# Kernel optimization log

Hardware: AMD Instinct MI355X
Metric: run time of the kernel (lower is better)

The kernel has to match this reference:

```python
import jax, jax.numpy as jnp
import numpy as np


def _hippo_scale_params(N, L):
    """Replicates HiPPOScale.__init__ for discretization='bilinear' (pure numpy)."""
    q = np.arange(N, dtype=np.float64)
    col, row = np.meshgrid(q, q)
    r = 2 * q + 1
    M = -(np.where(row >= col, r, 0) - np.diag(q))
    T = np.sqrt(np.diag(2 * q + 1))
    A = T @ M @ np.linalg.inv(T)          # (N, N)
    B = np.diag(T)                         # (N,)
    ts = np.arange(1, L + 1, dtype=np.float64)[:, None, None]  # (L,1,1)
    At = A[None] / ts                      # A / t, batched over t
    I = np.eye(N, dtype=np.float64)
    Mm = I[None] - 0.5 * At
    Nn = I[None] + 0.5 * At
    A_stacked = np.linalg.solve(Mm, Nn)                      # (L, N, N)
    Bt = B[None, :] / ts[:, 0, :]                             # (L, N)
    B_stacked = np.linalg.solve(Mm, Bt[..., None])[..., 0]    # (L, N)
    return A_stacked.astype(np.float32), B_stacked.astype(np.float32)


def setup_inputs() -> dict:
    N, L, Bsz = 64, 4096, 64
    key = jax.random.key(0)
    A_st, B_st = _hippo_scale_params(N, L)
    inputs = jax.random.normal(key, (L, Bsz), dtype=jnp.float32)
    return {
        "inputs": inputs,                       # (L, B)
        "A_stacked": jnp.asarray(A_st),         # (L, N, N)
        "B_stacked": jnp.asarray(B_st),         # (L, N)
    }


def reference(inputs, A_stacked, B_stacked):
    # u[t, b, :] = inputs[t, b] * B_stacked[t, :]   -> (L, B, N)
    u = inputs[..., None] * B_stacked[:, None, :]

    # x[t] = A[t] @ x[t-1] + u[t], x[-1] = 0  (time-varying linear recurrence).
    # The torch code computes this via a divide-and-conquer unroll; here we use
    # the equivalent parallel associative scan with elements (A, u) and
    # composition (A2@A1, A2@u1 + u2).
    def combine(e1, e2):
        a1, u1 = e1
        a2, u2 = e2
        a = jnp.matmul(a2, a1)                                  # (l, N, N)
        v = jnp.einsum('...ij,...bj->...bi', a2, u1) + u2       # (l, B, N)
        return (a, v)

    _, x = jax.lax.associative_scan(combine, (A_stacked, u))
    return x  # (L, B, N)
```

## Files before the change

kernel.cpp:

```cpp
#include <hip/hip_runtime.h>
#include <hip/hip_bf16.h>

#define TL 4096
#define NB 64
#define CH 8
#define CN 512
#define AS 72

typedef __attribute__((ext_vector_type(8))) short short8;
typedef __attribute__((ext_vector_type(4))) short short4v;
typedef __attribute__((ext_vector_type(4))) float floatx4;
typedef __attribute__((ext_vector_type(4))) unsigned int uint4v;

__device__ inline floatx4 mfma_bf16(short8 a, short8 b, floatx4 c) {
    return __builtin_amdgcn_mfma_f32_16x16x32_bf16(a, b, c, 0, 0, 0);
}

__device__ inline short bf16_rne(float x) {
    union { __hip_bfloat16 b; unsigned short s; } u;
    u.b = __float2bfloat16(x);
    return (short)u.s;
}

__device__ inline void split_bf16(float x, short& h, short& l) {
    h = bf16_rne(x);
    union { unsigned u; float f; } hv; hv.u = ((unsigned)(unsigned short)h) << 16;
    l = bf16_rne(x - hv.f);
}

__global__ __launch_bounds__(256, 2)
void hippo_phase1(const float* __restrict__ inp, const float* __restrict__ Ag,
                  const float* __restrict__ Bst,
                  unsigned* __restrict__ P32, float* __restrict__ VT)
{
    __shared__ short Ah[NB][AS], Al[NB][AS];
    __shared__ short SBh[NB][AS], SBl[NB][AS];
    __shared__ short VBh[NB][AS], VBl[NB][AS];
    __shared__ float btl[NB], itl[NB];

    const int tid  = threadIdx.x;
    const int c    = blockIdx.x;
    const int t0   = c * CH;
    const int w    = tid >> 6, lane = tid & 63;
    const int quad = lane >> 4, l15 = lane & 15;

#pragma unroll
    for (int q = 0; q < 16; ++q) {
        int f = tid + q * 256;
        int n = f >> 6, k = f & 63;
        SBh[n][k] = (n == k) ? (short)0x3F80 : (short)0;
        SBl[n][k] = 0; VBh[n][k] = 0; VBl[n][k] = 0;
    }

    float4 pre[4];
    {
        const float4* Ap = (const float4*)(Ag + (size_t)t0 * 4096);
#pragma unroll
        for (int q = 0; q < 4; ++q) pre[q] = Ap[tid + q * 256];
    }

    floatx4 accS[4], accV[4];

    for (int s = 0; s < CH; ++s) {
        int t = t0 + s;
#pragma unroll
        for (int q = 0; q < 4; ++q) {
            int f = tid + q * 256;
            int m = f >> 4, k0 = (f & 15) * 4;
            float vv[4] = {pre[q].x, pre[q].y, pre[q].z, pre[q].w};
            short4v h4, l4;
#pragma unroll
            for (int r = 0; r < 4; ++r) { short hh, ll; split_bf16(vv[r], hh, ll); h4[r]=hh; l4[r]=ll; }
            *(short4v*)&Ah[m][k0] = h4;
            *(short4v*)&Al[m][k0] = l4;
        }
        if (tid < 64) { btl[tid] = Bst[(size_t)t*64 + tid]; itl[tid] = inp[(size_t)t*64 + tid]; }
        if (s + 1 < CH) {
            const float4* Ap = (const float4*)(Ag + (size_t)(t+1) * 4096);
#pragma unroll
            for (int q = 0; q < 4; ++q) pre[q] = Ap[tid + q * 256];
        }
        __syncthreads();

#pragma unroll
        for (int ni = 0; ni < 4; ++ni) {
            float ib = itl[16*ni + l15];
#pragma unroll
            for (int r = 0; r < 4; ++r) {
                accS[ni][r] = 0.0f;
                accV[ni][r] = btl[16*w + 4*quad + r] * ib;
            }
        }
#pragma unroll
        for (int kc = 0; kc < 2; ++kc) {
            int ko = 32*kc + 8*quad;
            short8 aH = *(const short8*)&Ah[16*w + l15][ko];
            short8 aL = *(const short8*)&Al[16*w + l15][ko];
#pragma unroll
            for (int ni = 0; ni < 4; ++ni) {
                int n = 16*ni + l15;
                short8 sH = *(const short8*)&SBh[n][ko];
                short8 sL = *(const short8*)&SBl[n][ko];
                accS[ni] = mfma_bf16(aH, sH, accS[ni]);
                accS[ni] = mfma_bf16(aH, sL, accS[ni]);
                accS[ni] = mfma_bf16(aL, sH, accS[ni]);
                short8 vH = *(const short8*)&VBh[n][ko];
                short8 vL = *(const short8*)&VBl[n][ko];
                accV[ni] = mfma_bf16(aH, vH, accV[ni]);
                accV[ni] = mfma_bf16(aH, vL, accV[ni]);
                accV[ni] = mfma_bf16(aL, vH, accV[ni]);
            }
        }
        __syncthreads();

        if (s + 1 < CH) {
#pragma unroll
            for (int ni = 0; ni < 4; ++ni) {
                int cc = 16*ni + l15, r0 = 16*w + 4*quad;
                short4v h4, l4;
#pragma unroll
                for (int r = 0; r < 4; ++r) { short hh,ll; split_bf16(accS[ni][r],hh,ll); h4[r]=hh; l4[r]=ll; }
                *(short4v*)&SBh[cc][r0] = h4; *(short4v*)&SBl[cc][r0] = l4;
#pragma unroll
                for (int r = 0; r < 4; ++r) { short hh,ll; split_bf16(accV[ni][r],hh,ll); h4[r]=hh; l4[r]=ll; }
                *(short4v*)&VBh[cc][r0] = h4; *(short4v*)&VBl[cc][r0] = l4;
            }
        }
    }
    unsigned* po = P32 + (size_t)c * 4096;
#pragma unroll
    for (int ni = 0; ni < 4; ++ni) {
        int cc = 16*ni + l15, r0 = 16*w + 4*quad;
        *(floatx4*)(VT + (size_t)c*4096 + cc*64 + r0) = accV[ni];
#pragma unroll
        for (int r = 0; r < 4; ++r) {
            short hh, ll; split_bf16(accS[ni][r], hh, ll);
            po[(r0 + r)*64 + cc] = ((unsigned)(unsigned short)hh << 16) | (unsigned)(unsigned short)ll;
        }
    }
}

__global__ __launch_bounds__(256, 2)
void hippo_seqscan(unsigned* __restrict__ P32, float* __restrict__ VT,
                   int bstride, int off0, int estride)
{
    __shared__ short PAh[NB][AS], PAl[NB][AS];
    __shared__ short PBh[NB][AS], PBl[NB][AS];
    __shared__ short VBh[NB][AS], VBl[NB][AS];

    const int tid  = threadIdx.x;
    const int base = blockIdx.x * bstride + off0;
    const int w    = tid >> 6, lane = tid & 63;
    const int quad = lane >> 4, l15 = lane & 15;

    {
        const unsigned* p0 = P32 + (size_t)base * 4096;
        const float*    v0 = VT  + (size_t)base * 4096;
#pragma unroll
        for (int q = 0; q < 4; ++q) {
            int f = tid + q * 256;
            int k = f & 63, m0 = (f >> 6) * 4;
            uint4v pk = *(const uint4v*)(p0 + k * 64 + m0);
#pragma unroll
            for (int r = 0; r < 4; ++r) {
                PBh[m0 + r][k] = (short)(pk[r] >> 16);
                PBl[m0 + r][k] = (short)(pk[r] & 0xFFFFu);
            }
        }
#pragma unroll
        for (int q = 0; q < 4; ++q) {
            int f = tid + q * 256;
            int n = f >> 4, k0 = (f & 15) * 4;
            float4 vv = *(const float4*)(v0 + n * 64 + k0);
            float va[4] = {vv.x, vv.y, vv.z, vv.w};
            short4v vh4, vl4;
#pragma unroll
            for (int r = 0; r < 4; ++r) { short hh, ll; split_bf16(va[r], hh, ll); vh4[r]=hh; vl4[r]=ll; }
            *(short4v*)&VBh[n][k0] = vh4; *(short4v*)&VBl[n][k0] = vl4;
        }
    }

    uint4v preA[4]; float4 preV[4];
    {
        const unsigned* pc = P32 + (size_t)(base + estride) * 4096;
        const float*    vc = VT  + (size_t)(base + estride) * 4096;
#pragma unroll
        for (int q = 0; q < 4; ++q) {
            int f = tid + q * 256;
            int m = f >> 4, k0 = (f & 15) * 4;
            preA[q] = *(const uint4v*)(pc + m * 64 + k0);
        }
#pragma unroll
        for (int ni = 0; ni < 4; ++ni) {
            int cc = 16 * ni + l15, r0 = 16 * w + 4 * quad;
            preV[ni] = *(const float4*)(vc + cc * 64 + r0);
        }
    }

    for (int i = 1; i < 8; ++i) {
#pragma unroll
        for (int q = 0; q < 4; ++q) {
            int f = tid + q * 256;
            int m = f >> 4, k0 = (f & 15) * 4;
            short4v h4, l4;
#pragma unroll
            for (int r = 0; r < 4; ++r) { h4[r] = (short)(preA[q][r] >> 16); l4[r] = (short)(preA[q][r] & 0xFFFFu); }
            *(short4v*)&PAh[m][k0] = h4;
            *(short4v*)&PAl[m][k0] = l4;
        }
        floatx4 accP[4], accV[4];
#pragma unroll
        for (int ni = 0; ni < 4; ++ni) {
            accV[ni][0] = preV[ni].x; accV[ni][1] = preV[ni].y;
            accV[ni][2] = preV[ni].z; accV[ni][3] = preV[ni].w;
            accP[ni][0] = accP[ni][1] = accP[ni][2] = accP[ni][3] = 0.0f;
        }
        if (i + 1 < 8) {
            const unsigned* pc = P32 + (size_t)(base + (i + 1) * estride) * 4096;
            const float*    vc = VT  + (size_t)(base + (i + 1) * estride) * 4096;
#pragma unroll
            for (int q = 0; q < 4; ++q) {
                int f = tid + q * 256;
                int m = f >> 4, k0 = (f & 15) * 4;
                preA[q] = *(const uint4v*)(pc + m * 64 + k0);
            }
#pragma unroll
            for (int ni = 0; ni < 4; ++ni) {
                int cc = 16 * ni + l15, r0 = 16 * w + 4 * quad;
                preV[ni] = *(const float4*)(vc + cc * 64 + r0);
            }
        }
        __syncthreads();

#pragma unroll
        for (int kc = 0; kc < 2; ++kc) {
            int ko = 32 * kc + 8 * quad;
            short8 aH = *(const short8*)&PAh[16 * w + l15][ko];
            short8 aL = *(const short8*)&PAl[16 * w + l15][ko];
#pragma unroll
            for (int ni = 0; ni < 4; ++ni) {
                int n = 16 * ni + l15;
                short8 pH = *(const short8*)&PBh[n][ko];
                short8 pL = *(const short8*)&PBl[n][ko];
                accP[ni] = mfma_bf16(aH, pH, accP[ni]);
                accP[ni] = mfma_bf16(aH, pL, accP[ni]);
                accP[ni] = mfma_bf16(aL, pH, accP[ni]);
                short8 vH = *(const short8*)&VBh[n][ko];
                short8 vL = *(const short8*)&VBl[n][ko];
                accV[ni] = mfma_bf16(aH, vH, accV[ni]);
                accV[ni] = mfma_bf16(aH, vL, accV[ni]);
                accV[ni] = mfma_bf16(aL, vH, accV[ni]);
            }
        }
        __syncthreads();

        int idx = base + i * estride;
        unsigned* po = P32 + (size_t)idx * 4096;
#pragma unroll
        for (int ni = 0; ni < 4; ++ni) {
            int cc = 16 * ni + l15, r0 = 16 * w + 4 * quad;
            *(floatx4*)(VT + (size_t)idx * 4096 + cc * 64 + r0) = accV[ni];
            short4v h4, l4;
#pragma unroll
            for (int r = 0; r < 4; ++r) {
                short hh, ll; split_bf16(accP[ni][r], hh, ll);
                po[(r0 + r) * 64 + cc] = ((unsigned)(unsigned short)hh << 16) | (unsigned)(unsigned short)ll;
                h4[r] = hh; l4[r] = ll;
            }
            *(short4v*)&PBh[cc][r0] = h4; *(short4v*)&PBl[cc][r0] = l4;
#pragma unroll
            for (int r = 0; r < 4; ++r) { short hh,ll; split_bf16(accV[ni][r],hh,ll); h4[r]=hh; l4[r]=ll; }
            *(short4v*)&VBh[cc][r0] = h4; *(short4v*)&VBl[cc][r0] = l4;
        }
    }
}

__global__ __launch_bounds__(256, 2)
void hippo_s3(unsigned* __restrict__ P32, const float* __restrict__ VT)
{
    __shared__ short PAh[NB][AS], PAl[NB][AS];
    __shared__ short EBh[NB][AS], EBl[NB][AS];
    const int tid = threadIdx.x;
    const int w = tid >> 6, lane = tid & 63, quad = lane >> 4, l15 = lane & 15;

#pragma unroll
    for (int q = 0; q < 16; ++q) {
        int f = tid + q * 256; EBh[f >> 6][f & 63] = 0; EBl[f >> 6][f & 63] = 0;
    }
    for (int s = 0; s < 7; ++s) {
        int idx = 64 * s + 63;
        const unsigned* pc = P32 + (size_t)idx * 4096;
        const float*    vc = VT  + (size_t)idx * 4096;
#pragma unroll
        for (int q = 0; q < 4; ++q) {
            int f = tid + q * 256;
            int m = f >> 4, k0 = (f & 15) * 4;
            uint4v pk = *(const uint4v*)(pc + m * 64 + k0);
            short4v h4, l4;
#pragma unroll
            for (int r = 0; r < 4; ++r) { h4[r] = (short)(pk[r] >> 16); l4[r] = (short)(pk[r] & 0xFFFFu); }
            *(short4v*)&PAh[m][k0] = h4;
            *(short4v*)&PAl[m][k0] = l4;
        }
        floatx4 acc[4];
#pragma unroll
        for (int ni = 0; ni < 4; ++ni) {
            int cc = 16 * ni + l15, r0 = 16 * w + 4 * quad;
            float4 vv = *(const float4*)(vc + cc * 64 + r0);
            acc[ni][0] = vv.x; acc[ni][1] = vv.y; acc[ni][2] = vv.z; acc[ni][3] = vv.w;
        }
        __syncthreads();
#pragma unroll
        for (int kc = 0; kc < 2; ++kc) {
            int ko = 32 * kc + 8 * quad;
            short8 aH = *(const short8*)&PAh[16 * w + l15][ko];
            short8 aL = *(const short8*)&PAl[16 * w + l15][ko];
#pragma unroll
            for (int ni = 0; ni < 4; ++ni) {
                int n = 16 * ni + l15;
                short8 eH = *(const short8*)&EBh[n][ko];
                short8 eL = *(const short8*)&EBl[n][ko];
                acc[ni] = mfma_bf16(aH, eH, acc[ni]);
                acc[ni] = mfma_bf16(aH, eL, acc[ni]);
                acc[ni] = mfma_bf16(aL, eH, acc[ni]);
            }
        }
        __syncthreads();
        float* eo = (float*)(P32 + (size_t)idx * 4096);
#pragma unroll
        for (int ni = 0; ni < 4; ++ni) {
            int cc = 16 * ni + l15, r0 = 16 * w + 4 * quad;
            *(floatx4*)(eo + cc * 64 + r0) = acc[ni];
            short4v h4, l4;
#pragma unroll
            for (int r = 0; r < 4; ++r) { short hh,ll; split_bf16(acc[ni][r],hh,ll); h4[r]=hh; l4[r]=ll; }
            *(short4v*)&EBh[cc][r0] = h4; *(short4v*)&EBl[cc][r0] = l4;
        }
    }
}

__global__ __launch_bounds__(256, 2)
void hippo_phase3(const float* __restrict__ inp, const float* __restrict__ Ag,
                  const float* __restrict__ Bst, const unsigned* __restrict__ P32,
                  const float* __restrict__ VT, float* __restrict__ out)
{
    __shared__ short Ah[NB][AS], Al[NB][AS];
    __shared__ short XBh[NB][AS], XBl[NB][AS];
    __shared__ float btl[NB], itl[NB];

    const int tid = threadIdx.x, c = blockIdx.x, t0 = c * CH;
    const int w = tid>>6, lane = tid&63, quad = lane>>4, l15 = lane&15;
    const int sup = c >> 6, g = c >> 3, gi = g & 7, j = c & 7;

    float4 pre[4];
    {
        const float4* Ap = (const float4*)(Ag + (size_t)t0 * 4096);
#pragma unroll
        for (int q = 0; q < 4; ++q) pre[q] = Ap[tid + q * 256];
    }

    if (sup == 0) {
#pragma unroll
        for (int q = 0; q < 16; ++q) { int f = tid + q*256; XBh[f>>6][f&63] = 0; XBl[f>>6][f&63] = 0; }
    } else {
        const float* e = (const float*)(P32 + (size_t)(64*(sup-1) + 63) * 4096);
#pragma unroll
        for (int q = 0; q < 4; ++q) {
            int f = tid + q*256; int b = f>>4, k0 = (f&15)*4;
            float4 v = *(const float4*)(e + b*64 + k0);
            float va[4] = {v.x,v.y,v.z,v.w};
            short4v h4, l4;
#pragma unroll
            for (int r=0;r<4;++r){short hh,ll;split_bf16(va[r],hh,ll);h4[r]=hh;l4[r]=ll;}
            *(short4v*)&XBh[b][k0] = h4; *(short4v*)&XBl[b][k0] = l4;
        }
    }

    auto combine = [&](int idx) {
        const unsigned* pc = P32 + (size_t)idx * 4096;
        const float*    vc = VT  + (size_t)idx * 4096;
#pragma unroll
        for (int q = 0; q < 4; ++q) {
            int f = tid + q*256;
            int m = f >> 4, k0 = (f & 15) * 4;
            uint4v pk = *(const uint4v*)(pc + m * 64 + k0);
            short4v h4, l4;
#pragma unroll
            for (int r = 0; r < 4; ++r) { h4[r] = (short)(pk[r] >> 16); l4[r] = (short)(pk[r] & 0xFFFFu); }
            *(short4v*)&Ah[m][k0] = h4;
            *(short4v*)&Al[m][k0] = l4;
        }
        floatx4 acc[4];
#pragma unroll
        for (int ni = 0; ni < 4; ++ni) {
            int cc = 16*ni + l15, r0 = 16*w + 4*quad;
            float4 vv = *(const float4*)(vc + cc*64 + r0);
            acc[ni][0]=vv.x; acc[ni][1]=vv.y; acc[ni][2]=vv.z; acc[ni][3]=vv.w;
        }
        __syncthreads();
#pragma unroll
        for (int kc = 0; kc < 2; ++kc) {
            int ko = 32*kc + 8*quad;
            short8 aH = *(const short8*)&Ah[16*w + l15][ko];
            short8 aL = *(const short8*)&Al[16*w + l15][ko];
#pragma unroll
            for (int ni = 0; ni < 4; ++ni) {
                int n = 16*ni + l15;
                short8 xH = *(const short8*)&XBh[n][ko];
                short8 xL = *(const short8*)&XBl[n][ko];
                acc[ni] = mfma_bf16(aH, xH, acc[ni]);
                acc[ni] = mfma_bf16(aH, xL, acc[ni]);
                acc[ni] = mfma_bf16(aL, xH, acc[ni]);
            }
        }
        __syncthreads();
#pragma unroll
        for (int ni = 0; ni < 4; ++ni) {
            int cc = 16*ni + l15, r0 = 16*w + 4*quad;
            short4v h4, l4;
#pragma unroll
            for (int r=0;r<4;++r){short hh,ll;split_bf16(acc[ni][r],hh,ll);h4[r]=hh;l4[r]=ll;}
            *(short4v*)&XBh[cc][r0] = h4; *(short4v*)&XBl[cc][r0] = l4;
        }
    };
    if (gi) combine(8*g - 1);
    if (j)  combine(c - 1);

    floatx4 acc[4];
    for (int s = 0; s < CH; ++s) {
        int t = t0 + s;
#pragma unroll
        for (int q = 0; q < 4; ++q) {
            int f = tid + q*256; int m = f>>4, k0 = (f&15)*4;
            float vv[4] = {pre[q].x,pre[q].y,pre[q].z,pre[q].w};
            short4v h4, l4;
#pragma unroll
            for (int r=0;r<4;++r){short hh,ll;split_bf16(vv[r],hh,ll);h4[r]=hh;l4[r]=ll;}
            *(short4v*)&Ah[m][k0] = h4; *(short4v*)&Al[m][k0] = l4;
        }
        if (tid < 64) { btl[tid] = Bst[(size_t)t*64 + tid]; itl[tid] = inp[(size_t)t*64 + tid]; }
        if (s + 1 < CH) {
            const float4* Ap = (const float4*)(Ag + (size_t)(t+1) * 4096);
#pragma unroll
            for (int q = 0; q < 4; ++q) pre[q] = Ap[tid + q * 256];
        }
        __syncthreads();

#pragma unroll
        for (int ni = 0; ni < 4; ++ni) {
            float ib = itl[16*ni + l15];
#pragma unroll
            for (int r = 0; r < 4; ++r) acc[ni][r] = btl[16*w + 4*quad + r] * ib;
        }
#pragma unroll
        for (int kc = 0; kc < 2; ++kc) {
            int ko = 32*kc + 8*quad;
            short8 aH = *(const short8*)&Ah[16*w + l15][ko];
            short8 aL = *(const short8*)&Al[16*w + l15][ko];
#pragma unroll
            for (int ni = 0; ni < 4; ++ni) {
                int n = 16*ni + l15;
                short8 xH = *(const short8*)&XBh[n][ko];
                short8 xL = *(const short8*)&XBl[n][ko];
                acc[ni] = mfma_bf16(aH, xH, acc[ni]);
                acc[ni] = mfma_bf16(aH, xL, acc[ni]);
                acc[ni] = mfma_bf16(aL, xH, acc[ni]);
            }
        }
        __syncthreads();
#pragma unroll
        for (int ni = 0; ni < 4; ++ni) {
            int cc = 16*ni + l15, r0 = 16*w + 4*quad;
            *(floatx4*)(out + (size_t)t*4096 + cc*64 + r0) = acc[ni];
            if (s + 1 < CH) {
                short4v h4, l4;
#pragma unroll
                for (int r=0;r<4;++r){short hh,ll;split_bf16(acc[ni][r],hh,ll);h4[r]=hh;l4[r]=ll;}
                *(short4v*)&XBh[cc][r0] = h4; *(short4v*)&XBl[cc][r0] = l4;
            }
        }
    }
}

extern "C" void kernel_launch(void* const* d_in, const int* in_sizes, int n_in,
                              void* d_out, int out_size, void* d_ws, size_t ws_size,
                              hipStream_t stream)
{
    const float* inp = (const float*)d_in[0];
    const float* A   = (const float*)d_in[1];
    const float* Bst = (const float*)d_in[2];
    float* out = (float*)d_out;
    float* ws  = (float*)d_ws;

    unsigned* P32 = (unsigned*)ws;
    float*    VT  = ws + (size_t)CN * 4096;

    hippo_phase1<<<CN, 256, 0, stream>>>(inp, A, Bst, P32, VT);
    hippo_seqscan<<<64, 256, 0, stream>>>(P32, VT, 8, 0, 1);
    hippo_seqscan<<<8, 256, 0, stream>>>(P32, VT, 64, 7, 8);
    hippo_s3<<<1, 256, 0, stream>>>(P32, VT);
    hippo_phase3<<<CN, 256, 0, stream>>>(inp, A, Bst, P32, VT, out);
}
```

Baseline: 184.0 us.

## Use 2x2 warp tiling, skip identity step, prefetch B/input into registers

Each wave now computes a 32x32 output tile (two M blocks by two N blocks) instead of a 16x64 strip. This halves the redundant B-operand LDS reads per MFMA and lets the A fragments be reused across two column blocks. Phase 1 also skips the first step's multiply by the identity matrix: it loads A[t0] and the first u directly into the accumulators and starts the loop at s=1. The per-step B and input values are now prefetched into registers a step ahead instead of staged through shared memory by one wave. The cost is more live registers per thread and scattered scalar global loads for the initial A.

Measured after the change: 180.1 us. -2.2%, faster.

```diff
diff --git a/kernel.cpp b/kernel.cpp
--- a/kernel.cpp
+++ b/kernel.cpp
@@ -36,105 +36,164 @@
     __shared__ short Ah[NB][AS], Al[NB][AS];
     __shared__ short SBh[NB][AS], SBl[NB][AS];
     __shared__ short VBh[NB][AS], VBl[NB][AS];
-    __shared__ float btl[NB], itl[NB];
-
-    const int tid  = threadIdx.x;
-    const int c    = blockIdx.x;
-    const int t0   = c * CH;
-    const int w    = tid >> 6, lane = tid & 63;
+
+    const int tid = threadIdx.x;
+    const int c = blockIdx.x, t0 = c * CH;
+    const int w = tid >> 6, lane = tid & 63;
     const int quad = lane >> 4, l15 = lane & 15;
-
-#pragma unroll
-    for (int q = 0; q < 16; ++q) {
-        int f = tid + q * 256;
-        int n = f >> 6, k = f & 63;
-        SBh[n][k] = (n == k) ? (short)0x3F80 : (short)0;
-        SBl[n][k] = 0; VBh[n][k] = 0; VBl[n][k] = 0;
+    const int wm = w >> 1, wb = w & 1;
+    const int mr0 = 32*wm, br0 = 32*wb;
+
+    floatx4 accS[2][2], accV[2][2];
+
+    {
+        const float* A0 = Ag + (size_t)t0 * 4096;
+#pragma unroll
+        for (int mi = 0; mi < 2; ++mi) {
+            const int r0 = mr0 + 16*mi + 4*quad;
+            float bt[4];
+#pragma unroll
+            for (int r = 0; r < 4; ++r) bt[r] = Bst[(size_t)t0*64 + r0 + r];
+#pragma unroll
+            for (int ni = 0; ni < 2; ++ni) {
+                const int cc = br0 + 16*ni + l15;
+                const float ii = inp[(size_t)t0*64 + cc];
+#pragma unroll
+                for (int r = 0; r < 4; ++r) {
+                    accS[mi][ni][r] = A0[(size_t)(r0 + r)*64 + cc];
+                    accV[mi][ni][r] = bt[r] * ii;
+                }
+            }
+        }
     }
 
     float4 pre[4];
+    float preB[2][4], preI[2];
     {
-        const float4* Ap = (const float4*)(Ag + (size_t)t0 * 4096);
-#pragma unroll
-        for (int q = 0; q < 4; ++q) pre[q] = Ap[tid + q * 256];
-    }
-
-    floatx4 accS[4], accV[4];
-
-    for (int s = 0; s < CH; ++s) {
-        int t = t0 + s;
-#pragma unroll
-        for (int q = 0; q < 4; ++q) {
-            int f = tid + q * 256;
-            int m = f >> 4, k0 = (f & 15) * 4;
+        const float4* Ap = (const float4*)(Ag + (size_t)(t0+1) * 4096);
+#pragma unroll
+        for (int q = 0; q < 4; ++q) pre[q] = Ap[tid + q*256];
+#pragma unroll
+        for (int mi = 0; mi < 2; ++mi)
+#pragma unroll
+            for (int r = 0; r < 4; ++r)
+                preB[mi][r] = Bst[(size_t)(t0+1)*64 + mr0 + 16*mi + 4*quad + r];
+        preI[0] = inp[(size_t)(t0+1)*64 + br0 + l15];
+        preI[1] = inp[(size_t)(t0+1)*64 + br0 + 16 + l15];
+    }
+
+#pragma unroll
+    for (int mi = 0; mi < 2; ++mi)
+#pragma unroll
+    for (int ni = 0; ni < 2; ++ni) {
+        const int cc = br0 + 16*ni + l15, r0 = mr0 + 16*mi + 4*quad;
+        short4v h4, l4;
+#pragma unroll
+        for (int r = 0; r < 4; ++r) { short hh,ll; split_bf16(accS[mi][ni][r],hh,ll); h4[r]=hh; l4[r]=ll; }
+        *(short4v*)&SBh[cc][r0] = h4; *(short4v*)&SBl[cc][r0] = l4;
+#pragma unroll
+        for (int r = 0; r < 4; ++r) { short hh,ll; split_bf16(accV[mi][ni][r],hh,ll); h4[r]=hh; l4[r]=ll; }
+        *(short4v*)&VBh[cc][r0] = h4; *(short4v*)&VBl[cc][r0] = l4;
+    }
+
+    for (int s = 1; s < CH; ++s) {
+#pragma unroll
+        for (int q = 0; q < 4; ++q) {
+            int f = tid + q*256;
+            int m = f >> 4, k0 = (f & 15)*4;
             float vv[4] = {pre[q].x, pre[q].y, pre[q].z, pre[q].w};
             short4v h4, l4;
 #pragma unroll
-            for (int r = 0; r < 4; ++r) { short hh, ll; split_bf16(vv[r], hh, ll); h4[r]=hh; l4[r]=ll; }
-            *(short4v*)&Ah[m][k0] = h4;
-            *(short4v*)&Al[m][k0] = l4;
-        }
-        if (tid < 64) { btl[tid] = Bst[(size_t)t*64 + tid]; itl[tid] = inp[(size_t)t*64 + tid]; }
+            for (int r = 0; r < 4; ++r) { short hh,ll; split_bf16(vv[r],hh,ll); h4[r]=hh; l4[r]=ll; }
+            *(short4v*)&Ah[m][k0] = h4; *(short4v*)&Al[m][k0] = l4;
+        }
+        float bcur[2][4], icur[2];
+#pragma unroll
+        for (int mi=0;mi<2;++mi)
+#pragma unroll
+            for (int r=0;r<4;++r) bcur[mi][r] = preB[mi][r];
+        icur[0]=preI[0]; icur[1]=preI[1];
         if (s + 1 < CH) {
-            const float4* Ap = (const float4*)(Ag + (size_t)(t+1) * 4096);
-#pragma unroll
-            for (int q = 0; q < 4; ++q) pre[q] = Ap[tid + q * 256];
-        }
-        __syncthreads();
-
-#pragma unroll
-        for (int ni = 0; ni < 4; ++ni) {
-            float ib = itl[16*ni + l15];
-#pragma unroll
-            for (int r = 0; r < 4; ++r) {
-                accS[ni][r] = 0.0f;
-                accV[ni][r] = btl[16*w + 4*quad + r] * ib;
-            }
+            const int t1 = t0 + s + 1;
+            const float4* Ap = (const float4*)(Ag + (size_t)t1 * 4096);
+#pragma unroll
+            for (int q = 0; q < 4; ++q) pre[q] = Ap[tid + q*256];
+#pragma unroll
+            for (int mi=0;mi<2;++mi)
+#pragma unroll
+                for (int r=0;r<4;++r)
+                    preB[mi][r] = Bst[(size_t)t1*64 + mr0 + 16*mi + 4*quad + r];
+            preI[0] = inp[(size_t)t1*64 + br0 + l15];
+            preI[1] = inp[(size_t)t1*64 + br0 + 16 + l15];
+        }
+        __syncthreads();
+
+#pragma unroll
+        for (int mi=0;mi<2;++mi)
+#pragma unroll
+        for (int ni=0;ni<2;++ni)
+#pragma unroll
+        for (int r=0;r<4;++r) {
+            accS[mi][ni][r] = 0.0f;
+            accV[mi][ni][r] = bcur[mi][r] * icur[ni];
         }
 #pragma unroll
         for (int kc = 0; kc < 2; ++kc) {
-            int ko = 32*kc + 8*quad;
-            short8 aH = *(const short8*)&Ah[16*w + l15][ko];
-            short8 aL = *(const short8*)&Al[16*w + l15][ko];
-#pragma unroll
-            for (int ni = 0; ni < 4; ++ni) {
-                int n = 16*ni + l15;
+            const int ko = 32*kc + 8*quad;
+            short8 aH0 = *(const short8*)&Ah[mr0 + l15][ko];
+            short8 aL0 = *(const short8*)&Al[mr0 + l15][ko];
+            short8 aH1 = *(const short8*)&Ah[mr0 + 16 + l15][ko];
+            short8 aL1 = *(const short8*)&Al[mr0 + 16 + l15][ko];
+#pragma unroll
+            for (int ni = 0; ni < 2; ++ni) {
+                const int n = br0 + 16*ni + l15;
                 short8 sH = *(const short8*)&SBh[n][ko];
                 short8 sL = *(const short8*)&SBl[n][ko];
-                accS[ni] = mfma_bf16(aH, sH, accS[ni]);
-                accS[ni] = mfma_bf16(aH, sL, accS[ni]);
-                accS[ni] = mfma_bf16(aL, sH, accS[ni]);
                 short8 vH = *(const short8*)&VBh[n][ko];
                 short8 vL = *(const short8*)&VBl[n][ko];
-                accV[ni] = mfma_bf16(aH, vH, accV[ni]);
-                accV[ni] = mfma_bf16(aH, vL, accV[ni]);
-                accV[ni] = mfma_bf16(aL, vH, accV[ni]);
+                accS[0][ni] = mfma_bf16(aH0, sH, accS[0][ni]);
+                accS[0][ni] = mfma_bf16(aH0, sL, accS[0][ni]);
+                accS[0][ni] = mfma_bf16(aL0, sH, accS[0][ni]);
+                accS[1][ni] = mfma_bf16(aH1, sH, accS[1][ni]);
+                accS[1][ni] = mfma_bf16(aH1, sL, accS[1][ni]);
+                accS[1][ni] = mfma_bf16(aL1, sH, accS[1][ni]);
+                accV[0][ni] = mfma_bf16(aH0, vH, accV[0][ni]);
+                accV[0][ni] = mfma_bf16(aH0, vL, accV[0][ni]);
+                accV[0][ni] = mfma_bf16(aL0, vH, accV[0][ni]);
+                accV[1][ni] = mfma_bf16(aH1, vH, accV[1][ni]);
+                accV[1][ni] = mfma_bf16(aH1, vL, accV[1][ni]);
+                accV[1][ni] = mfma_bf16(aL1, vH, accV[1][ni]);
             }
         }
         __syncthreads();
 
         if (s + 1 < CH) {
 #pragma unroll
-            for (int ni = 0; ni < 4; ++ni) {
-                int cc = 16*ni + l15, r0 = 16*w + 4*quad;
+            for (int mi = 0; mi < 2; ++mi)
+#pragma unroll
+            for (int ni = 0; ni < 2; ++ni) {
+                const int cc = br0 + 16*ni + l15, r0 = mr0 + 16*mi + 4*quad;
                 short4v h4, l4;
 #pragma unroll
-                for (int r = 0; r < 4; ++r) { short hh,ll; split_bf16(accS[ni][r],hh,ll); h4[r]=hh; l4[r]=ll; }
+                for (int r = 0; r < 4; ++r) { short hh,ll; split_bf16(accS[mi][ni][r],hh,ll); h4[r]=hh; l4[r]=ll; }
                 *(short4v*)&SBh[cc][r0] = h4; *(short4v*)&SBl[cc][r0] = l4;
 #pragma unroll
-                for (int r = 0; r < 4; ++r) { short hh,ll; split_bf16(accV[ni][r],hh,ll); h4[r]=hh; l4[r]=ll; }
+                for (int r = 0; r < 4; ++r) { short hh,ll; split_bf16(accV[mi][ni][r],hh,ll); h4[r]=hh; l4[r]=ll; }
                 *(short4v*)&VBh[cc][r0] = h4; *(short4v*)&VBl[cc][r0] = l4;
             }
         }
     }
+
     unsigned* po = P32 + (size_t)c * 4096;
 #pragma unroll
-    for (int ni = 0; ni < 4; ++ni) {
-        int cc = 16*ni + l15, r0 = 16*w + 4*quad;
-        *(floatx4*)(VT + (size_t)c*4096 + cc*64 + r0) = accV[ni];
+    for (int mi = 0; mi < 2; ++mi)
+#pragma unroll
+    for (int ni = 0; ni < 2; ++ni) {
+        const int cc = br0 + 16*ni + l15, r0 = mr0 + 16*mi + 4*quad;
+        *(floatx4*)(VT + (size_t)c*4096 + cc*64 + r0) = accV[mi][ni];
 #pragma unroll
         for (int r = 0; r < 4; ++r) {
-            short hh, ll; split_bf16(accS[ni][r], hh, ll);
+            short hh, ll; split_bf16(accS[mi][ni][r], hh, ll);
             po[(r0 + r)*64 + cc] = ((unsigned)(unsigned short)hh << 16) | (unsigned)(unsigned short)ll;
         }
     }
@@ -148,10 +207,12 @@
     __shared__ short PBh[NB][AS], PBl[NB][AS];
     __shared__ short VBh[NB][AS], VBl[NB][AS];
 
-    const int tid  = threadIdx.x;
+    const int tid = threadIdx.x;
     const int base = blockIdx.x * bstride + off0;
-    const int w    = tid >> 6, lane = tid & 63;
+    const int w = tid >> 6, lane = tid & 63;
     const int quad = lane >> 4, l15 = lane & 15;
+    const int wm = w >> 1, wb = w & 1;
+    const int mr0 = 32*wm, br0 = 32*wb;
 
     {
         const unsigned* p0 = P32 + (size_t)base * 4096;
@@ -180,7 +241,7 @@
         }
     }
 
-    uint4v preA[4]; float4 preV[4];
+    uint4v preA[4]; float4 preV[2][2];
     {
         const unsigned* pc = P32 + (size_t)(base + estride) * 4096;
         const float*    vc = VT  + (size_t)(base + estride) * 4096;
@@ -191,9 +252,11 @@
             preA[q] = *(const uint4v*)(pc + m * 64 + k0);
         }
 #pragma unroll
-        for (int ni = 0; ni < 4; ++ni) {
-            int cc = 16 * ni + l15, r0 = 16 * w + 4 * quad;
-            preV[ni] = *(const float4*)(vc + cc * 64 + r0);
+        for (int mi = 0; mi < 2; ++mi)
+#pragma unroll
+        for (int ni = 0; ni < 2; ++ni) {
+            const int cc = br0 + 16*ni + l15, r0 = mr0 + 16*mi + 4*quad;
+            preV[mi][ni] = *(const float4*)(vc + cc * 64 + r0);
         }
     }
 
@@ -208,12 +271,14 @@
             *(short4v*)&PAh[m][k0] = h4;
             *(short4v*)&PAl[m][k0] = l4;
         }
-        floatx4 accP[4], accV[4];
-#pragma unroll
-        for (int ni = 0; ni < 4; ++ni) {
-            accV[ni][0] = preV[ni].x; accV[ni][1] = preV[ni].y;
-            accV[ni][2] = preV[ni].z; accV[ni][3] = preV[ni].w;
-            accP[ni][0] = accP[ni][1] = accP[ni][2] = accP[ni][3] = 0.0f;
+        floatx4 accP[2][2], accV[2][2];
+#pragma unroll
+        for (int mi = 0; mi < 2; ++mi)
+#pragma unroll
+        for (int ni = 0; ni < 2; ++ni) {
+            accV[mi][ni][0] = preV[mi][ni].x; accV[mi][ni][1] = preV[mi][ni].y;
+            accV[mi][ni][2] = preV[mi][ni].z; accV[mi][ni][3] = preV[mi][ni].w;
+            accP[mi][ni][0]=accP[mi][ni][1]=accP[mi][ni][2]=accP[mi][ni][3]=0.0f;
         }
         if (i + 1 < 8) {
             const unsigned* pc = P32 + (size_t)(base + (i + 1) * estride) * 4096;
@@ -225,51 +290,63 @@
                 preA[q] = *(const uint4v*)(pc + m * 64 + k0);
             }
 #pragma unroll
-            for (int ni = 0; ni < 4; ++ni) {
-                int cc = 16 * ni + l15, r0 = 16 * w + 4 * quad;
-                preV[ni] = *(const float4*)(vc + cc * 64 + r0);
+            for (int mi = 0; mi < 2; ++mi)
+#pragma unroll
+            for (int ni = 0; ni < 2; ++ni) {
+                const int cc = br0 + 16*ni + l15, r0 = mr0 + 16*mi + 4*quad;
+                preV[mi][ni] = *(const float4*)(vc + cc * 64 + r0);
             }
         }
         __syncthreads();
 
 #pragma unroll
         for (int kc = 0; kc < 2; ++kc) {
-            int ko = 32 * kc + 8 * quad;
-            short8 aH = *(const short8*)&PAh[16 * w + l15][ko];
-            short8 aL = *(const short8*)&PAl[16 * w + l15][ko];
-#pragma unroll
-            for (int ni = 0; ni < 4; ++ni) {
-                int n = 16 * ni + l15;
+            const int ko = 32*kc + 8*quad;
+            short8 aH0 = *(const short8*)&PAh[mr0 + l15][ko];
+            short8 aL0 = *(const short8*)&PAl[mr0 + l15][ko];
+            short8 aH1 = *(const short8*)&PAh[mr0 + 16 + l15][ko];
+            short8 aL1 = *(const short8*)&PAl[mr0 + 16 + l15][ko];
+#pragma unroll
+            for (int ni = 0; ni < 2; ++ni) {
+                const int n = br0 + 16*ni + l15;
                 short8 pH = *(const short8*)&PBh[n][ko];
                 short8 pL = *(const short8*)&PBl[n][ko];
-                accP[ni] = mfma_bf16(aH, pH, accP[ni]);
-                accP[ni] = mfma_bf16(aH, pL, accP[ni]);
-                accP[ni] = mfma_bf16(aL, pH, accP[ni]);
                 short8 vH = *(const short8*)&VBh[n][ko];
                 short8 vL = *(const short8*)&VBl[n][ko];
-                accV[ni] = mfma_bf16(aH, vH, accV[ni]);
-                accV[ni] = mfma_bf16(aH, vL, accV[ni]);
-                accV[ni] = mfma_bf16(aL, vH, accV[ni]);
-            }
-        }
-        __syncthreads();
-
-        int idx = base + i * estride;
+                accP[0][ni] = mfma_bf16(aH0, pH, accP[0][ni]);
+                accP[0][ni] = mfma_bf16(aH0, pL, accP[0][ni]);
+                accP[0][ni] = mfma_bf16(aL0, pH, accP[0][ni]);
+                accP[1][ni] = mfma_bf16(aH1, pH, accP[1][ni]);
+                accP[1][ni] = mfma_bf16(aH1, pL, accP[1][ni]);
+                accP[1][ni] = mfma_bf16(aL1, pH, accP[1][ni]);
+                accV[0][ni] = mfma_bf16(aH0, vH, accV[0][ni]);
+                accV[0][ni] = mfma_bf16(aH0, vL, accV[0][ni]);
+                accV[0][ni] = mfma_bf16(aL0, vH, accV[0][ni]);
+                accV[1][ni] = mfma_bf16(aH1, vH, accV[1][ni]);
+                accV[1][ni] = mfma_bf16(aH1, vL, accV[1][ni]);
+                accV[1][ni] = mfma_bf16(aL1, vH, accV[1][ni]);
+            }
+        }
+        __syncthreads();
+
+        const int idx = base + i * estride;
         unsigned* po = P32 + (size_t)idx * 4096;
 #pragma unroll
-        for (int ni = 0; ni < 4; ++ni) {
-            int cc = 16 * ni + l15, r0 = 16 * w + 4 * quad;
-            *(floatx4*)(VT + (size_t)idx * 4096 + cc * 64 + r0) = accV[ni];
+        for (int mi = 0; mi < 2; ++mi)
+#pragma unroll
+        for (int ni = 0; ni < 2; ++ni) {
+            const int cc = br0 + 16*ni + l15, r0 = mr0 + 16*mi + 4*quad;
+            *(floatx4*)(VT + (size_t)idx * 4096 + cc * 64 + r0) = accV[mi][ni];
             short4v h4, l4;
 #pragma unroll
             for (int r = 0; r < 4; ++r) {
-                short hh, ll; split_bf16(accP[ni][r], hh, ll);
+                short hh, ll; split_bf16(accP[mi][ni][r], hh, ll);
                 po[(r0 + r) * 64 + cc] = ((unsigned)(unsigned short)hh << 16) | (unsigned)(unsigned short)ll;
                 h4[r] = hh; l4[r] = ll;
             }
             *(short4v*)&PBh[cc][r0] = h4; *(short4v*)&PBl[cc][r0] = l4;
 #pragma unroll
-            for (int r = 0; r < 4; ++r) { short hh,ll; split_bf16(accV[ni][r],hh,ll); h4[r]=hh; l4[r]=ll; }
+            for (int r = 0; r < 4; ++r) { short hh,ll; split_bf16(accV[mi][ni][r],hh,ll); h4[r]=hh; l4[r]=ll; }
             *(short4v*)&VBh[cc][r0] = h4; *(short4v*)&VBl[cc][r0] = l4;
         }
     }
@@ -282,13 +359,15 @@
     __shared__ short EBh[NB][AS], EBl[NB][AS];
     const int tid = threadIdx.x;
     const int w = tid >> 6, lane = tid & 63, quad = lane >> 4, l15 = lane & 15;
+    const int wm = w >> 1, wb = w & 1;
+    const int mr0 = 32*wm, br0 = 32*wb;
 
 #pragma unroll
     for (int q = 0; q < 16; ++q) {
         int f = tid + q * 256; EBh[f >> 6][f & 63] = 0; EBl[f >> 6][f & 63] = 0;
     }
     for (int s = 0; s < 7; ++s) {
-        int idx = 64 * s + 63;
+        const int idx = 64 * s + 63;
         const unsigned* pc = P32 + (size_t)idx * 4096;
         const float*    vc = VT  + (size_t)idx * 4096;
 #pragma unroll
@@ -302,38 +381,47 @@
             *(short4v*)&PAh[m][k0] = h4;
             *(short4v*)&PAl[m][k0] = l4;
         }
-        floatx4 acc[4];
-#pragma unroll
-        for (int ni = 0; ni < 4; ++ni) {
-            int cc = 16 * ni + l15, r0 = 16 * w + 4 * quad;
+        floatx4 acc[2][2];
+#pragma unroll
+        for (int mi = 0; mi < 2; ++mi)
+#pragma unroll
+        for (int ni = 0; ni < 2; ++ni) {
+            const int cc = br0 + 16*ni + l15, r0 = mr0 + 16*mi + 4*quad;
             float4 vv = *(const float4*)(vc + cc * 64 + r0);
-            acc[ni][0] = vv.x; acc[ni][1] = vv.y; acc[ni][2] = vv.z; acc[ni][3] = vv.w;
+            acc[mi][ni][0]=vv.x; acc[mi][ni][1]=vv.y; acc[mi][ni][2]=vv.z; acc[mi][ni][3]=vv.w;
         }
         __syncthreads();
 #pragma unroll
         for (int kc = 0; kc < 2; ++kc) {
-            int ko = 32 * kc + 8 * quad;
-            short8 aH = *(const short8*)&PAh[16 * w + l15][ko];
-            short8 aL = *(const short8*)&PAl[16 * w + l15][ko];
-#pragma unroll
-            for (int ni = 0; ni < 4; ++ni) {
-                int n = 16 * ni + l15;
+            const int ko = 32*kc + 8*quad;
+            short8 aH0 = *(const short8*)&PAh[mr0 + l15][ko];
+            short8 aL0 = *(const short8*)&PAl[mr0 + l15][ko];
+            short8 aH1 = *(const short8*)&PAh[mr0 + 16 + l15][ko];
+            short8 aL1 = *(const short8*)&PAl[mr0 + 16 + l15][ko];
+#pragma unroll
+            for (int ni = 0; ni < 2; ++ni) {
+                const int n = br0 + 16*ni + l15;
                 short8 eH = *(const short8*)&EBh[n][ko];
                 short8 eL = *(const short8*)&EBl[n][ko];
-                acc[ni] = mfma_bf16(aH, eH, acc[ni]);
-                acc[ni] = mfma_bf16(aH, eL, acc[ni]);
-                acc[ni] = mfma_bf16(aL, eH, acc[ni]);
+                acc[0][ni] = mfma_bf16(aH0, eH, acc[0][ni]);
+                acc[0][ni] = mfma_bf16(aH0, eL, acc[0][ni]);
+                acc[0][ni] = mfma_bf16(aL0, eH, acc[0][ni]);
+                acc[1][ni] = mfma_bf16(aH1, eH, acc[1][ni]);
+                acc[1][ni] = mfma_bf16(aH1, eL, acc[1][ni]);
+                acc[1][ni] = mfma_bf16(aL1, eH, acc[1][ni]);
             }
         }
         __syncthreads();
         float* eo = (float*)(P32 + (size_t)idx * 4096);
 #pragma unroll
-        for (int ni = 0; ni < 4; ++ni) {
-            int cc = 16 * ni + l15, r0 = 16 * w + 4 * quad;
-            *(floatx4*)(eo + cc * 64 + r0) = acc[ni];
-            short4v h4, l4;
-#pragma unroll
-            for (int r = 0; r < 4; ++r) { short hh,ll; split_bf16(acc[ni][r],hh,ll); h4[r]=hh; l4[r]=ll; }
+        for (int mi = 0; mi < 2; ++mi)
+#pragma unroll
+        for (int ni = 0; ni < 2; ++ni) {
+            const int cc = br0 + 16*ni + l15, r0 = mr0 + 16*mi + 4*quad;
+            *(floatx4*)(eo + cc * 64 + r0) = acc[mi][ni];
+            short4v h4, l4;
+#pragma unroll
+            for (int r = 0; r < 4; ++r) { short hh,ll; split_bf16(acc[mi][ni][r],hh,ll); h4[r]=hh; l4[r]=ll; }
             *(short4v*)&EBh[cc][r0] = h4; *(short4v*)&EBl[cc][r0] = l4;
         }
     }
@@ -346,10 +434,11 @@
 {
     __shared__ short Ah[NB][AS], Al[NB][AS];
     __shared__ short XBh[NB][AS], XBl[NB][AS];
-    __shared__ float btl[NB], itl[NB];
 
     const int tid = threadIdx.x, c = blockIdx.x, t0 = c * CH;
-    const int w = tid>>6, lane = tid&63, quad = lane>>4, l15 = lane&15;
+    const int w = tid >> 6, lane = tid & 63, quad = lane >> 4, l15 = lane & 15;
+    const int wm = w >> 1, wb = w & 1;
+    const int mr0 = 32*wm, br0 = 32*wb;
     const int sup = c >> 6, g = c >> 3, gi = g & 7, j = c & 7;
 
     float4 pre[4];
@@ -390,45 +479,63 @@
             *(short4v*)&Ah[m][k0] = h4;
             *(short4v*)&Al[m][k0] = l4;
         }
-        floatx4 acc[4];
-#pragma unroll
-        for (int ni = 0; ni < 4; ++ni) {
-            int cc = 16*ni + l15, r0 = 16*w + 4*quad;
+        floatx4 acc[2][2];
+#pragma unroll
+        for (int mi = 0; mi < 2; ++mi)
+#pragma unroll
+        for (int ni = 0; ni < 2; ++ni) {
+            const int cc = br0 + 16*ni + l15, r0 = mr0 + 16*mi + 4*quad;
             float4 vv = *(const float4*)(vc + cc*64 + r0);
-            acc[ni][0]=vv.x; acc[ni][1]=vv.y; acc[ni][2]=vv.z; acc[ni][3]=vv.w;
+            acc[mi][ni][0]=vv.x; acc[mi][ni][1]=vv.y; acc[mi][ni][2]=vv.z; acc[mi][ni][3]=vv.w;
         }
         __syncthreads();
 #pragma unroll
         for (int kc = 0; kc < 2; ++kc) {
-            int ko = 32*kc + 8*quad;
-            short8 aH = *(const short8*)&Ah[16*w + l15][ko];
-            short8 aL = *(const short8*)&Al[16*w + l15][ko];
-#pragma unroll
-            for (int ni = 0; ni < 4; ++ni) {
-                int n = 16*ni + l15;
+            const int ko = 32*kc + 8*quad;
+            short8 aH0 = *(const short8*)&Ah[mr0 + l15][ko];
+            short8 aL0 = *(const short8*)&Al[mr0 + l15][ko];
+            short8 aH1 = *(const short8*)&Ah[mr0 + 16 + l15][ko];
+            short8 aL1 = *(const short8*)&Al[mr0 + 16 + l15][ko];
+#pragma unroll
+            for (int ni = 0; ni < 2; ++ni) {
+                const int n = br0 + 16*ni + l15;
                 short8 xH = *(const short8*)&XBh[n][ko];
                 short8 xL = *(const short8*)&XBl[n][ko];
-                acc[ni] = mfma_bf16(aH, xH, acc[ni]);
-                acc[ni] = mfma_bf16(aH, xL, acc[ni]);
-                acc[ni] = mfma_bf16(aL, xH, acc[ni]);
-            }
-        }
-        __syncthreads();
-#pragma unroll
-        for (int ni = 0; ni < 4; ++ni) {
-            int cc = 16*ni + l15, r0 = 16*w + 4*quad;
-            short4v h4, l4;
-#pragma unroll
-            for (int r=0;r<4;++r){short hh,ll;split_bf16(acc[ni][r],hh,ll);h4[r]=hh;l4[r]=ll;}
+                acc[0][ni] = mfma_bf16(aH0, xH, acc[0][ni]);
+                acc[0][ni] = mfma_bf16(aH0, xL, acc[0][ni]);
+                acc[0][ni] = mfma_bf16(aL0, xH, acc[0][ni]);
+                acc[1][ni] = mfma_bf16(aH1, xH, acc[1][ni]);
+                acc[1][ni] = mfma_bf16(aH1, xL, acc[1][ni]);
+                acc[1][ni] = mfma_bf16(aL1, xH, acc[1][ni]);
+            }
+        }
+        __syncthreads();
+#pragma unroll
+        for (int mi = 0; mi < 2; ++mi)
+#pragma unroll
+        for (int ni = 0; ni < 2; ++ni) {
+            const int cc = br0 + 16*ni + l15, r0 = mr0 + 16*mi + 4*quad;
+            short4v h4, l4;
+#pragma unroll
+            for (int r=0;r<4;++r){short hh,ll;split_bf16(acc[mi][ni][r],hh,ll);h4[r]=hh;l4[r]=ll;}
             *(short4v*)&XBh[cc][r0] = h4; *(short4v*)&XBl[cc][r0] = l4;
         }
     };
     if (gi) combine(8*g - 1);
     if (j)  combine(c - 1);
 
-    floatx4 acc[4];
+    float preB[2][4], preI[2];
+#pragma unroll
+    for (int mi = 0; mi < 2; ++mi)
+#pragma unroll
+        for (int r = 0; r < 4; ++r)
+            preB[mi][r] = Bst[(size_t)t0*64 + mr0 + 16*mi + 4*quad + r];
+    preI[0] = inp[(size_t)t0*64 + br0 + l15];
+    preI[1] = inp[(size_t)t0*64 + br0 + 16 + l15];
+
+    floatx4 acc[2][2];
     for (int s = 0; s < CH; ++s) {
-        int t = t0 + s;
+        const int t = t0 + s;
 #pragma unroll
         for (int q = 0; q < 4; ++q) {
             int f = tid + q*256; int m = f>>4, k0 = (f&15)*4;
@@ -438,44 +545,64 @@
             for (int r=0;r<4;++r){short hh,ll;split_bf16(vv[r],hh,ll);h4[r]=hh;l4[r]=ll;}
             *(short4v*)&Ah[m][k0] = h4; *(short4v*)&Al[m][k0] = l4;
         }
-        if (tid < 64) { btl[tid] = Bst[(size_t)t*64 + tid]; itl[tid] = inp[(size_t)t*64 + tid]; }
+        float bcur[2][4], icur[2];
+#pragma unroll
+        for (int mi=0;mi<2;++mi)
+#pragma unroll
+            for (int r=0;r<4;++r) bcur[mi][r] = preB[mi][r];
+        icur[0]=preI[0]; icur[1]=preI[1];
         if (s + 1 < CH) {
-            const float4* Ap = (const float4*)(Ag + (size_t)(t+1) * 4096);
+            const int t1 = t + 1;
+            const float4* Ap = (const float4*)(Ag + (size_t)t1 * 4096);
 #pragma unroll
             for (int q = 0; q < 4; ++q) pre[q] = Ap[tid + q * 256];
-        }
-        __syncthreads();
-
-#pragma unroll
-        for (int ni = 0; ni < 4; ++ni) {
-            float ib = itl[16*ni + l15];
-#pragma unroll
-            for (int r = 0; r < 4; ++r) acc[ni][r] = btl[16*w + 4*quad + r] * ib;
-        }
+#pragma unroll
+            for (int mi=0;mi<2;++mi)
+#pragma unroll
+                for (int r=0;r<4;++r)
+                    preB[mi][r] = Bst[(size_t)t1*64 + mr0 + 16*mi + 4*quad + r];
+            preI[0] = inp[(size_t)t1*64 + br0 + l15];
+            preI[1] = inp[(size_t)t1*64 + br0 + 16 + l15];
+        }
+        __syncthreads();
+
+#pragma unroll
+        for (int mi=0;mi<2;++mi)
+#pragma unroll
+        for (int ni=0;ni<2;++ni)
+#pragma unroll
+        for (int r=0;r<4;++r) acc[mi][ni][r] = bcur[mi][r] * icur[ni];
 #pragma unroll
         for (int kc = 0; kc < 2; ++kc) {
-            int ko = 32*kc + 8*quad;
-            short8 aH = *(const short8*)&Ah[16*w + l15][ko];
-            short8 aL = *(const short8*)&Al[16*w + l15][ko];
-#pragma unroll
-            for (int ni = 0; ni < 4; ++ni) {
-                int n = 16*ni + l15;
+            const int ko = 32*kc + 8*quad;
+            short8 aH0 = *(const short8*)&Ah[mr0 + l15][ko];
+            short8 aL0 = *(const short8*)&Al[mr0 + l15][ko];
+            short8 aH1 = *(const short8*)&Ah[mr0 + 16 + l15][ko];
+            short8 aL1 = *(const short8*)&Al[mr0 + 16 + l15][ko];
+#pragma unroll
+            for (int ni = 0; ni < 2; ++ni) {
+                const int n = br0 + 16*ni + l15;
                 short8 xH = *(const short8*)&XBh[n][ko];
                 short8 xL = *(const short8*)&XBl[n][ko];
-                acc[ni] = mfma_bf16(aH, xH, acc[ni]);
-                acc[ni] = mfma_bf16(aH, xL, acc[ni]);
-                acc[ni] = mfma_bf16(aL, xH, acc[ni]);
-            }
-        }
-        __syncthreads();
-#pragma unroll
-        for (int ni = 0; ni < 4; ++ni) {
-            int cc = 16*ni + l15, r0 = 16*w + 4*quad;
-            *(floatx4*)(out + (size_t)t*4096 + cc*64 + r0) = acc[ni];
+                acc[0][ni] = mfma_bf16(aH0, xH, acc[0][ni]);
+                acc[0][ni] = mfma_bf16(aH0, xL, acc[0][ni]);
+                acc[0][ni] = mfma_bf16(aL0, xH, acc[0][ni]);
+                acc[1][ni] = mfma_bf16(aH1, xH, acc[1][ni]);
+                acc[1][ni] = mfma_bf16(aH1, xL, acc[1][ni]);
+                acc[1][ni] = mfma_bf16(aL1, xH, acc[1][ni]);
+            }
+        }
+        __syncthreads();
+#pragma unroll
+        for (int mi = 0; mi < 2; ++mi)
+#pragma unroll
+        for (int ni = 0; ni < 2; ++ni) {
+            const int cc = br0 + 16*ni + l15, r0 = mr0 + 16*mi + 4*quad;
+            *(floatx4*)(out + (size_t)t*4096 + cc*64 + r0) = acc[mi][ni];
             if (s + 1 < CH) {
                 short4v h4, l4;
 #pragma unroll
-                for (int r=0;r<4;++r){short hh,ll;split_bf16(acc[ni][r],hh,ll);h4[r]=hh;l4[r]=ll;}
+                for (int r=0;r<4;++r){short hh,ll;split_bf16(acc[mi][ni][r],hh,ll);h4[r]=hh;l4[r]=ll;}
                 *(short4v*)&XBh[cc][r0] = h4; *(short4v*)&XBl[cc][r0] = l4;
             }
         }
```
